# Kernel optimization log

Hardware: AMD Instinct MI355X
Metric: run time of the kernel (lower is better)

## Reference

```python
import jax, jax.numpy as jnp
import numpy as np

B, N, M, K = 4, 16384, 16384, 16   # batch, points, centers, neighbors
C, O, G = 64, 64, 8                # in_planes, out_planes, group


def setup_inputs() -> dict:
    key = jax.random.key(0)
    ks = jax.random.split(key, 16)
    r = lambda i, sh, s=1.0: jax.random.normal(ks[i], sh, jnp.float32) * s
    return dict(
        center_pos=r(0, (B, M, 3)),
        center_fea=r(1, (B, C, M)),
        pos=r(2, (B, N, 3)),
        fea=r(3, (B, C, N)),
        idx=jax.random.randint(ks[4], (B, M, K), 0, N, jnp.int32),
        # linear q/k/v
        Wq=r(5, (C, O), 0.05), bq=jnp.zeros((O,), jnp.float32),
        Wk=r(6, (C, O), 0.05), bk=jnp.zeros((O,), jnp.float32),
        Wv=r(7, (C, O), 0.05), bv=jnp.zeros((O,), jnp.float32),
        # center_pos_encode: conv1x1(3->O, no bias) + folded BN (scale,shift) + relu + conv1x1(O->O)
        cpe_w1=r(8, (3, O), 0.05), cpe_s=jnp.ones((O,), jnp.float32), cpe_b=jnp.zeros((O,), jnp.float32),
        cpe_w2=r(9, (O, O), 0.05), cpe_b2=jnp.zeros((O,), jnp.float32),
        # pos_encode (Conv2d 1x1 == per-point linear)
        pe_w1=r(10, (3, O), 0.05), pe_s=jnp.ones((O,), jnp.float32), pe_b=jnp.zeros((O,), jnp.float32),
        pe_w2=r(11, (O, O), 0.05), pe_b2=jnp.zeros((O,), jnp.float32),
        # weight_encode (O -> G)
        we_w1=r(12, (O, G), 0.05), we_s=jnp.ones((G,), jnp.float32), we_b=jnp.zeros((G,), jnp.float32),
        we_w2=r(13, (G, G), 0.05), we_b2=jnp.zeros((G,), jnp.float32),
    )


def _mlp2(x, w1, s, b, w2, b2):
    # conv1x1(no bias) -> inference BatchNorm folded to (scale, shift) -> ReLU -> conv1x1(+bias)
    h = jax.nn.relu(x @ w1 * s + b)
    return h @ w2 + b2


def reference(center_pos, center_fea, pos, fea, idx,
              Wq, bq, Wk, bk, Wv, bv,
              cpe_w1, cpe_s, cpe_b, cpe_w2, cpe_b2,
              pe_w1, pe_s, pe_b, pe_w2, pe_b2,
              we_w1, we_s, we_b, we_w2, we_b2):
    x_q = center_fea.transpose(0, 2, 1) @ Wq + bq        # [B,M,O]
    ft = fea.transpose(0, 2, 1)                          # [B,N,C]
    x_k = ft @ Wk + bk                                   # [B,N,O]
    x_v = ft @ Wv + bv                                   # [B,N,O]

    gather = jax.vmap(lambda a, i: a[i])                 # per-batch irregular gather
    nk = gather(x_k, idx)                                # [B,M,K,O]
    nv = gather(x_v, idx)                                # [B,M,K,O]
    npos = gather(pos, idx) - center_pos[:, :, None, :]  # [B,M,K,3] relative coords

    cpr = _mlp2(center_pos, cpe_w1, cpe_s, cpe_b, cpe_w2, cpe_b2)  # [B,M,O]
    pr = _mlp2(npos, pe_w1, pe_s, pe_b, pe_w2, pe_b2)              # [B,M,K,O]

    r_qk = nk - x_q[:, :, None, :] + cpr[:, :, None, :]  # [B,M,K,O]
    v = nv + pr                                          # [B,M,K,O]

    w = _mlp2(r_qk, we_w1, we_s, we_b, we_w2, we_b2)     # [B,M,K,G]
    w = jax.nn.softmax(w, axis=2)                        # softmax over neighbors

    v = v.reshape(B, M, K, G, O // G)
    out = jnp.einsum('bmkgi,bmkg->bmgi', v, w).reshape(B, M, O)
    return out.transpose(0, 2, 1)                        # [B,O,M]
```

## Files before the change

kernel.cpp:

```cpp
#include <hip/hip_runtime.h>
#include <hip/hip_bf16.h>

typedef unsigned short u16;
typedef __attribute__((ext_vector_type(8))) __bf16 bf8v;
typedef __attribute__((ext_vector_type(4))) float f32x4;
typedef __attribute__((ext_vector_type(4))) unsigned uint4v;

#define B_ 4
#define N_ 16384
#define M_ 16384
#define K_ 16
#define C_ 64
#define O_ 64
#define G_ 8

__device__ __forceinline__ float bf2f(u16 x){
  union { unsigned u; float f; } v; v.u = ((unsigned)x) << 16; return v.f;
}
__device__ __forceinline__ u16 f2bf(float f){
  union { float f; unsigned u; } v; v.f = f;
  unsigned u = v.u;
  return (u16)((u + 0x7FFFu + ((u >> 16) & 1u)) >> 16);
}

__global__ __launch_bounds__(256) void pre_kernel(
    const float* __restrict__ center_pos, const float* __restrict__ center_fea,
    const float* __restrict__ fea,
    const float* __restrict__ Wq, const float* __restrict__ bq,
    const float* __restrict__ Wk, const float* __restrict__ bk,
    const float* __restrict__ Wv, const float* __restrict__ bv,
    const float* __restrict__ cpe_w1, const float* __restrict__ cpe_s, const float* __restrict__ cpe_b,
    const float* __restrict__ cpe_w2, const float* __restrict__ cpe_b2,
    const float* __restrict__ we_w1,
    u16* __restrict__ xk, u16* __restrict__ xv, float* __restrict__ qw)
{
  int tid = threadIdx.x;
  int blk = blockIdx.x;
  __shared__ u16 sWT[128*72];
  __shared__ u16 sOut[64*136];
  __shared__ float sMisc[784];

  int l = tid & 63, w = tid >> 6, c = l & 15, q = l >> 4;

  if (blk < 1024) {
    int P0 = blk * 64; int b = P0 >> 14; int n0 = P0 & (N_-1);
    for (int e = tid; e < 8192; e += 256){
      int k = e >> 7, col = e & 127;
      float v = (col < 64) ? Wk[k*64 + col] : Wv[k*64 + (col-64)];
      sWT[col*72 + k] = f2bf(v);
    }
    if (tid < 128) sMisc[tid] = (tid < 64) ? bk[tid] : bv[tid-64];
    __syncthreads();

    int mIdx = n0 + w*16 + c;
    const float* fb = fea + (long)b*C_*N_;
    bf8v af[2];
    #pragma unroll
    for (int ks=0; ks<2; ks++){
      union { bf8v v; u16 s[8]; } ua;
      #pragma unroll
      for (int j=0; j<8; j++)
        ua.s[j] = f2bf(fb[(long)(ks*32 + q*8 + j)*N_ + mIdx]);
      af[ks] = ua.v;
    }

    f32x4 acc[8];
    #pragma unroll
    for (int t=0; t<8; t++){
      float bias = sMisc[16*t + c];
      f32x4 a_ = {bias, bias, bias, bias};
      bf8v b0 = *(const bf8v*)&sWT[(16*t + c)*72 + q*8];
      bf8v b1 = *(const bf8v*)&sWT[(16*t + c)*72 + 32 + q*8];
      a_ = __builtin_amdgcn_mfma_f32_16x16x32_bf16(af[0], b0, a_, 0,0,0);
      a_ = __builtin_amdgcn_mfma_f32_16x16x32_bf16(af[1], b1, a_, 0,0,0);
      acc[t] = a_;
    }

    #pragma unroll
    for (int t=0; t<8; t++)
      #pragma unroll
      for (int r=0; r<4; r++)
        sOut[(w*16 + q*4 + r)*136 + 16*t + c] = f2bf(acc[t][r]);
    __syncthreads();

    #pragma unroll
    for (int rep=0; rep<4; rep++){
      int chunk = rep*256 + tid;
      int pt = chunk >> 4, c8i = chunk & 15;
      uint4v val = *(const uint4v*)&sOut[pt*136 + c8i*8];
      int col8 = c8i*8;
      long row = (long)P0 + pt;
      if (col8 < 64) *(uint4v*)(xk + row*64 + col8)      = val;
      else           *(uint4v*)(xv + row*64 + (col8-64)) = val;
    }
  } else {
    int P0 = (blk - 1024) * 64; int b = P0 >> 14; int m0 = P0 & (M_-1);
    for (int e = tid; e < 512; e += 256) sMisc[e] = we_w1[e];
    if (tid < 64){
      float sc = cpe_s[tid];
      sMisc[512+tid] = cpe_w1[tid]      * sc;
      sMisc[576+tid] = cpe_w1[64+tid]   * sc;
      sMisc[640+tid] = cpe_w1[128+tid]  * sc;
      sMisc[704+tid] = cpe_b[tid];
    }
    __syncthreads();

    {
      int k = tid >> 1, g0 = (tid & 1)*4;
      const float* brow = (k < 64) ? (cpe_w2 + k*64) : (Wq + (k-64)*64);
      float sgn = (k < 64) ? 1.f : -1.f;
      float aw[4] = {0.f,0.f,0.f,0.f};
      for (int o=0; o<64; o++){
        float bo = brow[o]*sgn;
        #pragma unroll
        for (int gg=0; gg<4; gg++) aw[gg] += bo * sMisc[o*8 + g0+gg];
      }
      #pragma unroll
      for (int gg=0; gg<4; gg++) sWT[(g0+gg)*136 + k] = f2bf(aw[gg]);
    }
    for (int e = tid; e < 1088; e += 256) sWT[1088 + e] = 0;
    if (tid < 8){
      float s = 0.f;
      for (int o=0; o<64; o++) s += (cpe_b2[o] - bq[o]) * sMisc[o*8 + tid];
      sMisc[768 + tid] = s;
    }
    __syncthreads();

    int pg = P0 + w*16 + c;
    int mIdx = m0 + w*16 + c;
    long c3 = (long)pg * 3;
    float cp0 = center_pos[c3], cp1 = center_pos[c3+1], cp2 = center_pos[c3+2];
    bf8v ah[2], acf[2];
    #pragma unroll
    for (int ks=0; ks<2; ks++){
      union { bf8v v; u16 s[8]; } ua;
      #pragma unroll
      for (int j=0; j<8; j++){
        int h = ks*32 + q*8 + j;
        float hv = cp0*sMisc[512+h] + cp1*sMisc[576+h] + cp2*sMisc[640+h] + sMisc[704+h];
        ua.s[j] = f2bf(fmaxf(hv, 0.f));
      }
      ah[ks] = ua.v;
    }
    const float* cfb = center_fea + (long)b*C_*M_;
    #pragma unroll
    for (int ks=0; ks<2; ks++){
      union { bf8v v; u16 s[8]; } ua;
      #pragma unroll
      for (int j=0; j<8; j++)
        ua.s[j] = f2bf(cfb[(long)(ks*32 + q*8 + j)*M_ + mIdx]);
      acf[ks] = ua.v;
    }

    float cinit = (c < 8) ? sMisc[768 + c] : 0.f;
    f32x4 aq = {cinit, cinit, cinit, cinit};
    {
      bf8v b0 = *(const bf8v*)&sWT[c*136 + q*8];
      bf8v b1 = *(const bf8v*)&sWT[c*136 + 32 + q*8];
      bf8v b2 = *(const bf8v*)&sWT[c*136 + 64 + q*8];
      bf8v b3 = *(const bf8v*)&sWT[c*136 + 96 + q*8];
      aq = __builtin_amdgcn_mfma_f32_16x16x32_bf16(ah[0], b0, aq, 0,0,0);
      aq = __builtin_amdgcn_mfma_f32_16x16x32_bf16(ah[1], b1, aq, 0,0,0);
      aq = __builtin_amdgcn_mfma_f32_16x16x32_bf16(acf[0], b2, aq, 0,0,0);
      aq = __builtin_amdgcn_mfma_f32_16x16x32_bf16(acf[1], b3, aq, 0,0,0);
    }
    __syncthreads();
    if (c < 8){
      #pragma unroll
      for (int r=0; r<4; r++) sMisc[(w*16 + q*4 + r)*8 + c] = aq[r];
    }
    __syncthreads();
    for (int e = tid; e < 512; e += 256)
      qw[(long)P0*8 + e] = sMisc[e];
  }
}

__global__ __launch_bounds__(256) void attn_kernel(
    const float* __restrict__ center_pos, const float* __restrict__ pos,
    const int* __restrict__ idx,
    const float* __restrict__ pe_w1, const float* __restrict__ pe_s, const float* __restrict__ pe_b,
    const float* __restrict__ pe_w2, const float* __restrict__ pe_b2,
    const float* __restrict__ we_w1, const float* __restrict__ we_s, const float* __restrict__ we_b,
    const float* __restrict__ we_w2, const float* __restrict__ we_b2,
    const u16* __restrict__ xk, const u16* __restrict__ xv, const float* __restrict__ qw,
    float* __restrict__ out)
{
  int tid = threadIdx.x;
  __shared__ float s_w1f[192];
  __shared__ float s_pb[64];
  __shared__ float s_ws[8], s_wb[8], s_wb2[8];
  __shared__ float s_ww2[64];
  __shared__ float s_pb2[64];
  __shared__ u16  s_vt[4*16*72];
  __shared__ float s_tile[32*66];

  if (tid < 64){
    float sc = pe_s[tid];
    s_w1f[tid]     = pe_w1[tid]*sc;
    s_w1f[64+tid]  = pe_w1[64+tid]*sc;
    s_w1f[128+tid] = pe_w1[128+tid]*sc;
    s_pb[tid]  = pe_b[tid];
    s_pb2[tid] = pe_b2[tid];
    s_ww2[tid] = we_w2[tid];
  }
  if (tid >= 64 && tid < 72){
    int g = tid-64;
    s_ws[g]=we_s[g]; s_wb[g]=we_b[g]; s_wb2[g]=we_b2[g];
  }
  __syncthreads();

  int w = tid >> 6, l = tid & 63, c = l & 15, q = l >> 4, c8 = c & 7, qb = l & 48;

  bf8v pw2f[4][2], ww1f[2];
  {
    union { bf8v v; u16 s[8]; } u_;
    #pragma unroll
    for (int t=0;t<4;t++)
      #pragma unroll
      for (int ks=0;ks<2;ks++){
        #pragma unroll
        for (int j=0;j<8;j++) u_.s[j] = f2bf(pe_w2[(ks*32 + q*8 + j)*64 + t*16 + c]);
        pw2f[t][ks] = u_.v;
      }
    #pragma unroll
    for (int ks=0;ks<2;ks++){
      #pragma unroll
      for (int j=0;j<8;j++) u_.s[j] = (c < 8) ? f2bf(we_w1[(ks*32 + q*8 + j)*8 + c]) : (u16)0;
      ww1f[ks] = u_.v;
    }
  }
  float ws_c = s_ws[c8], wb_c = s_wb[c8], wb2_c = s_wb2[c8];
  float w2col[8];
  #pragma unroll
  for (int g=0; g<8; g++) w2col[g] = s_ww2[g*8 + c8];
  float pb2t[4];
  #pragma unroll
  for (int t=0;t<4;t++) pb2t[t] = s_pb2[t*16 + c];

  int pbase = blockIdx.x * 32;
  int b = pbase >> 14;
  long xkb = (long)b * N_ * 64;
  u16* vt = s_vt + w*(16*72);

  int p = pbase + w*8;
  int iv = idx[(long)p*16 + c];
  float qpv = qw[(long)p*8 + c8];
  long c30 = (long)p*3;
  float cp0 = center_pos[c30], cp1 = center_pos[c30+1], cp2 = center_pos[c30+2];

  #pragma unroll 1
  for (int i = 0; i < 8; i++){
    long pr3 = ((long)b*N_ + iv) * 3;
    float np0 = pos[pr3]   - cp0;
    float np1 = pos[pr3+1] - cp1;
    float np2 = pos[pr3+2] - cp2;
    const u16* krow = xk + xkb + (long)iv * 64;
    bf8v ka0 = *(const bf8v*)(krow + q*8);
    bf8v ka1 = *(const bf8v*)(krow + 32 + q*8);
    const u16* vrow = xv + xkb + (long)iv * 64;
    uint4v va0 = *(const uint4v*)(vrow + q*8);
    uint4v va1 = *(const uint4v*)(vrow + 32 + q*8);

    int pn = p + ((i < 7) ? 1 : 0);
    int iv_n = idx[(long)pn*16 + c];
    float qpv_n = qw[(long)pn*8 + c8];
    long c3n = (long)pn*3;
    float cpn0 = center_pos[c3n], cpn1 = center_pos[c3n+1], cpn2 = center_pos[c3n+2];

    *(uint4v*)&vt[c*72 + q*8]      = va0;
    *(uint4v*)&vt[c*72 + 32 + q*8] = va1;

    bf8v h1f[2];
    {
      union { bf8v v; u16 s[8]; } hu;
      #pragma unroll
      for (int ks=0;ks<2;ks++){
        #pragma unroll
        for (int j=0;j<8;j++){
          int o = ks*32 + q*8 + j;
          float hv = np0*s_w1f[o] + np1*s_w1f[64+o] + np2*s_w1f[128+o] + s_pb[o];
          hu.s[j] = f2bf(fmaxf(hv, 0.f));
        }
        h1f[ks] = hu.v;
      }
    }

    f32x4 h2a = {qpv, qpv, qpv, qpv};
    h2a = __builtin_amdgcn_mfma_f32_16x16x32_bf16(ka0, ww1f[0], h2a, 0, 0, 0);
    h2a = __builtin_amdgcn_mfma_f32_16x16x32_bf16(ka1, ww1f[1], h2a, 0, 0, 0);

    f32x4 prA[4];
    #pragma unroll
    for (int t=0;t<4;t++){
      f32x4 z = {0.f,0.f,0.f,0.f};
      z = __builtin_amdgcn_mfma_f32_16x16x32_bf16(h1f[0], pw2f[t][0], z, 0, 0, 0);
      z = __builtin_amdgcn_mfma_f32_16x16x32_bf16(h1f[1], pw2f[t][1], z, 0, 0, 0);
      prA[t] = z;
    }

    float h2r[4];
    #pragma unroll
    for (int r=0;r<4;r++) h2r[r] = fmaxf(h2a[r]*ws_c + wb_c, 0.f);
    float wl[4] = {wb2_c, wb2_c, wb2_c, wb2_c};
    #pragma unroll
    for (int g=0; g<8; g++){
      float wg = w2col[g];
      #pragma unroll
      for (int r=0;r<4;r++)
        wl[r] += __shfl(h2r[r], qb | g, 64) * wg;
    }
    float mx = fmaxf(fmaxf(wl[0],wl[1]), fmaxf(wl[2],wl[3]));
    mx = fmaxf(mx, __shfl_xor(mx, 16, 64));
    mx = fmaxf(mx, __shfl_xor(mx, 32, 64));
    float e[4];
    #pragma unroll
    for (int r=0;r<4;r++) e[r] = exp2f((wl[r]-mx)*1.44269504f);
    float sm = e[0]+e[1]+e[2]+e[3];
    sm += __shfl_xor(sm, 16, 64);
    sm += __shfl_xor(sm, 32, 64);
    float rn = 1.0f / sm;
    #pragma unroll
    for (int r=0;r<4;r++) e[r] *= rn;

    float ov[4] = {0.f,0.f,0.f,0.f};
    int ch = c >> 3;
    #pragma unroll
    for (int r=0;r<4;r++){
      #pragma unroll
      for (int t=0;t<4;t++){
        float wv_ = __shfl(e[r], qb | (t*2 + ch), 64);
        float nvv = bf2f(vt[(q*4+r)*72 + t*16 + c]);
        ov[t] += (prA[t][r] + nvv) * wv_;
      }
    }
    #pragma unroll
    for (int t=0;t<4;t++){
      ov[t] += __shfl_xor(ov[t], 16, 64);
      ov[t] += __shfl_xor(ov[t], 32, 64);
      ov[t] += pb2t[t];
    }
    float selv = ov[0];
    selv = (q==1) ? ov[1] : selv;
    selv = (q==2) ? ov[2] : selv;
    selv = (q==3) ? ov[3] : selv;
    s_tile[(w*8+i)*66 + l] = selv;

    p = pn; iv = iv_n; qpv = qpv_n; cp0 = cpn0; cp1 = cpn1; cp2 = cpn2;
  }
  __syncthreads();

  int o0 = tid >> 5, pt = tid & 31;
  int m0 = pbase & (M_-1);
  long outb = ((long)b*64) * M_ + m0 + pt;
  #pragma unroll
  for (int ii=0; ii<8; ii++){
    int o = o0*8 + ii;
    out[outb + (long)o*M_] = s_tile[pt*66 + o];
  }
}

extern "C" void kernel_launch(void* const* d_in, const int* in_sizes, int n_in,
                              void* d_out, int out_size, void* d_ws, size_t ws_size,
                              hipStream_t stream) {
  const float* center_pos = (const float*)d_in[0];
  const float* center_fea = (const float*)d_in[1];
  const float* pos        = (const float*)d_in[2];
  const float* fea        = (const float*)d_in[3];
  const int*   idx        = (const int*)d_in[4];
  const float* Wq = (const float*)d_in[5];   const float* bq = (const float*)d_in[6];
  const float* Wk = (const float*)d_in[7];   const float* bk = (const float*)d_in[8];
  const float* Wv = (const float*)d_in[9];   const float* bv = (const float*)d_in[10];
  const float* cpe_w1 = (const float*)d_in[11]; const float* cpe_s = (const float*)d_in[12];
  const float* cpe_b  = (const float*)d_in[13]; const float* cpe_w2 = (const float*)d_in[14];
  const float* cpe_b2 = (const float*)d_in[15];
  const float* pe_w1 = (const float*)d_in[16]; const float* pe_s = (const float*)d_in[17];
  const float* pe_b  = (const float*)d_in[18]; const float* pe_w2 = (const float*)d_in[19];
  const float* pe_b2 = (const float*)d_in[20];
  const float* we_w1 = (const float*)d_in[21]; const float* we_s = (const float*)d_in[22];
  const float* we_b  = (const float*)d_in[23]; const float* we_w2 = (const float*)d_in[24];
  const float* we_b2 = (const float*)d_in[25];

  const size_t SZ = (size_t)B_*N_*64;
  u16* xk = (u16*)d_ws;
  u16* xv = xk + SZ;
  float* qwp = (float*)(xv + SZ);
  float* outp = (float*)d_out;

  hipLaunchKernelGGL(pre_kernel, dim3(2048), dim3(256), 0, stream,
      center_pos, center_fea, fea, Wq, bq, Wk, bk, Wv, bv,
      cpe_w1, cpe_s, cpe_b, cpe_w2, cpe_b2, we_w1, xk, xv, qwp);
  hipLaunchKernelGGL(attn_kernel, dim3(2048), dim3(256), 0, stream,
      center_pos, pos, idx, pe_w1, pe_s, pe_b, pe_w2, pe_b2,
      we_w1, we_s, we_b, we_w2, we_b2, xk, xv, qwp, outp);
}
```

Before: 225.8 us.

## Split pre-kernel, coalesce feature loads via LDS, and process two centers per attention iteration

```diff
diff --git a/kernel.cpp b/kernel.cpp
--- a/kernel.cpp
+++ b/kernel.cpp
@@ -22,160 +22,179 @@
   unsigned u = v.u;
   return (u16)((u + 0x7FFFu + ((u >> 16) & 1u)) >> 16);
 }
-
-__global__ __launch_bounds__(256) void pre_kernel(
-    const float* __restrict__ center_pos, const float* __restrict__ center_fea,
+union pk2 { unsigned u; _Float16 h[2]; };
+__device__ __forceinline__ unsigned packh(float a, float b){
+  pk2 p; p.h[0] = (_Float16)a; p.h[1] = (_Float16)b; return p.u;
+}
+
+__global__ __launch_bounds__(256) void setup_kernel(
+    const float* __restrict__ Wq, const float* __restrict__ bq,
+    const float* __restrict__ cpe_w2, const float* __restrict__ cpe_b2,
+    const float* __restrict__ we_w1,
+    u16* __restrict__ bw, float* __restrict__ cinit)
+{
+  __shared__ float sWe[512];
+  int tid = threadIdx.x;
+  for (int e = tid; e < 512; e += 256) sWe[e] = we_w1[e];
+  __syncthreads();
+  int k = tid >> 1, g0 = (tid & 1)*4;
+  const float* brow = (k < 64) ? (cpe_w2 + k*64) : (Wq + (k-64)*64);
+  float sgn = (k < 64) ? 1.f : -1.f;
+  float aw[4] = {0.f,0.f,0.f,0.f};
+  for (int o = 0; o < 64; o++){
+    float bo = brow[o]*sgn;
+    #pragma unroll
+    for (int gg=0; gg<4; gg++) aw[gg] += bo * sWe[o*8 + g0+gg];
+  }
+  #pragma unroll
+  for (int gg=0; gg<4; gg++) bw[(g0+gg)*136 + k] = f2bf(aw[gg]);
+  for (int e = tid; e < 2176; e += 256){
+    int r = e / 136, cc = e % 136;
+    if (r >= 8 || cc >= 128) bw[e] = 0;
+  }
+  if (tid < 8){
+    float s = 0.f;
+    for (int o = 0; o < 64; o++) s += (cpe_b2[o] - bq[o]) * sWe[o*8 + tid];
+    cinit[tid] = s;
+  }
+}
+
+__global__ __launch_bounds__(256) void kv_kernel(
     const float* __restrict__ fea,
-    const float* __restrict__ Wq, const float* __restrict__ bq,
     const float* __restrict__ Wk, const float* __restrict__ bk,
     const float* __restrict__ Wv, const float* __restrict__ bv,
+    u16* __restrict__ xk, u16* __restrict__ xv)
+{
+  __shared__ u16 sWT[128*72];
+  __shared__ u16 sA[64*72];
+  __shared__ u16 sOut[64*136];
+  __shared__ float sBias[128];
+  int tid = threadIdx.x;
+  int l = tid & 63, w = tid >> 6, c = l & 15, q = l >> 4;
+  int P0 = blockIdx.x * 64; int b = P0 >> 14; int n0 = P0 & (N_-1);
+  const float* fb = fea + (long)b*C_*N_;
+
+  #pragma unroll
+  for (int pp = 0; pp < 4; pp++){
+    int k = pp*16 + (tid >> 4);
+    int nf = (tid & 15)*4;
+    f32x4 v = *(const f32x4*)&fb[(long)k*N_ + n0 + nf];
+    sA[(nf+0)*72+k] = f2bf(v[0]); sA[(nf+1)*72+k] = f2bf(v[1]);
+    sA[(nf+2)*72+k] = f2bf(v[2]); sA[(nf+3)*72+k] = f2bf(v[3]);
+  }
+  for (int e = tid; e < 8192; e += 256){
+    int k = e >> 7, col = e & 127;
+    float v = (col < 64) ? Wk[k*64 + col] : Wv[k*64 + (col-64)];
+    sWT[col*72 + k] = f2bf(v);
+  }
+  if (tid < 128) sBias[tid] = (tid < 64) ? bk[tid] : bv[tid-64];
+  __syncthreads();
+
+  bf8v af0 = *(const bf8v*)&sA[(w*16+c)*72 + q*8];
+  bf8v af1 = *(const bf8v*)&sA[(w*16+c)*72 + 32 + q*8];
+
+  f32x4 acc[8];
+  #pragma unroll
+  for (int t = 0; t < 8; t++){
+    float bias = sBias[16*t + c];
+    f32x4 a_ = {bias, bias, bias, bias};
+    bf8v b0 = *(const bf8v*)&sWT[(16*t + c)*72 + q*8];
+    bf8v b1 = *(const bf8v*)&sWT[(16*t + c)*72 + 32 + q*8];
+    a_ = __builtin_amdgcn_mfma_f32_16x16x32_bf16(af0, b0, a_, 0,0,0);
+    a_ = __builtin_amdgcn_mfma_f32_16x16x32_bf16(af1, b1, a_, 0,0,0);
+    acc[t] = a_;
+  }
+  #pragma unroll
+  for (int t = 0; t < 8; t++)
+    #pragma unroll
+    for (int r = 0; r < 4; r++)
+      sOut[(w*16 + q*4 + r)*136 + 16*t + c] = f2bf(acc[t][r]);
+  __syncthreads();
+
+  #pragma unroll
+  for (int rep = 0; rep < 4; rep++){
+    int chunk = rep*256 + tid;
+    int pt = chunk >> 4, c8i = chunk & 15;
+    uint4v val = *(const uint4v*)&sOut[pt*136 + c8i*8];
+    int col8 = c8i*8;
+    long row = (long)P0 + pt;
+    if (col8 < 64) *(uint4v*)(xk + row*64 + col8)      = val;
+    else           *(uint4v*)(xv + row*64 + (col8-64)) = val;
+  }
+}
+
+__global__ __launch_bounds__(256) void qc_kernel(
+    const float* __restrict__ center_pos, const float* __restrict__ center_fea,
     const float* __restrict__ cpe_w1, const float* __restrict__ cpe_s, const float* __restrict__ cpe_b,
-    const float* __restrict__ cpe_w2, const float* __restrict__ cpe_b2,
-    const float* __restrict__ we_w1,
-    u16* __restrict__ xk, u16* __restrict__ xv, float* __restrict__ qw)
+    const u16* __restrict__ bw, const float* __restrict__ cinit,
+    float* __restrict__ qw)
 {
+  __shared__ u16 sBw[16*136];
+  __shared__ u16 sA[64*72];
+  __shared__ float sW1[256];
+  __shared__ float sQ[512];
   int tid = threadIdx.x;
-  int blk = blockIdx.x;
-  __shared__ u16 sWT[128*72];
-  __shared__ u16 sOut[64*136];
-  __shared__ float sMisc[784];
-
   int l = tid & 63, w = tid >> 6, c = l & 15, q = l >> 4;
-
-  if (blk < 1024) {
-    int P0 = blk * 64; int b = P0 >> 14; int n0 = P0 & (N_-1);
-    for (int e = tid; e < 8192; e += 256){
-      int k = e >> 7, col = e & 127;
-      float v = (col < 64) ? Wk[k*64 + col] : Wv[k*64 + (col-64)];
-      sWT[col*72 + k] = f2bf(v);
-    }
-    if (tid < 128) sMisc[tid] = (tid < 64) ? bk[tid] : bv[tid-64];
-    __syncthreads();
-
-    int mIdx = n0 + w*16 + c;
-    const float* fb = fea + (long)b*C_*N_;
-    bf8v af[2];
-    #pragma unroll
-    for (int ks=0; ks<2; ks++){
-      union { bf8v v; u16 s[8]; } ua;
-      #pragma unroll
-      for (int j=0; j<8; j++)
-        ua.s[j] = f2bf(fb[(long)(ks*32 + q*8 + j)*N_ + mIdx]);
-      af[ks] = ua.v;
-    }
-
-    f32x4 acc[8];
-    #pragma unroll
-    for (int t=0; t<8; t++){
-      float bias = sMisc[16*t + c];
-      f32x4 a_ = {bias, bias, bias, bias};
-      bf8v b0 = *(const bf8v*)&sWT[(16*t + c)*72 + q*8];
-      bf8v b1 = *(const bf8v*)&sWT[(16*t + c)*72 + 32 + q*8];
-      a_ = __builtin_amdgcn_mfma_f32_16x16x32_bf16(af[0], b0, a_, 0,0,0);
-      a_ = __builtin_amdgcn_mfma_f32_16x16x32_bf16(af[1], b1, a_, 0,0,0);
-      acc[t] = a_;
-    }
-
-    #pragma unroll
-    for (int t=0; t<8; t++)
-      #pragma unroll
-      for (int r=0; r<4; r++)
-        sOut[(w*16 + q*4 + r)*136 + 16*t + c] = f2bf(acc[t][r]);
-    __syncthreads();
-
-    #pragma unroll
-    for (int rep=0; rep<4; rep++){
-      int chunk = rep*256 + tid;
-      int pt = chunk >> 4, c8i = chunk & 15;
-      uint4v val = *(const uint4v*)&sOut[pt*136 + c8i*8];
-      int col8 = c8i*8;
-      long row = (long)P0 + pt;
-      if (col8 < 64) *(uint4v*)(xk + row*64 + col8)      = val;
-      else           *(uint4v*)(xv + row*64 + (col8-64)) = val;
-    }
-  } else {
-    int P0 = (blk - 1024) * 64; int b = P0 >> 14; int m0 = P0 & (M_-1);
-    for (int e = tid; e < 512; e += 256) sMisc[e] = we_w1[e];
-    if (tid < 64){
-      float sc = cpe_s[tid];
-      sMisc[512+tid] = cpe_w1[tid]      * sc;
-      sMisc[576+tid] = cpe_w1[64+tid]   * sc;
-      sMisc[640+tid] = cpe_w1[128+tid]  * sc;
-      sMisc[704+tid] = cpe_b[tid];
-    }
-    __syncthreads();
-
-    {
-      int k = tid >> 1, g0 = (tid & 1)*4;
-      const float* brow = (k < 64) ? (cpe_w2 + k*64) : (Wq + (k-64)*64);
-      float sgn = (k < 64) ? 1.f : -1.f;
-      float aw[4] = {0.f,0.f,0.f,0.f};
-      for (int o=0; o<64; o++){
-        float bo = brow[o]*sgn;
-        #pragma unroll
-        for (int gg=0; gg<4; gg++) aw[gg] += bo * sMisc[o*8 + g0+gg];
-      }
-      #pragma unroll
-      for (int gg=0; gg<4; gg++) sWT[(g0+gg)*136 + k] = f2bf(aw[gg]);
-    }
-    for (int e = tid; e < 1088; e += 256) sWT[1088 + e] = 0;
-    if (tid < 8){
-      float s = 0.f;
-      for (int o=0; o<64; o++) s += (cpe_b2[o] - bq[o]) * sMisc[o*8 + tid];
-      sMisc[768 + tid] = s;
-    }
-    __syncthreads();
-
-    int pg = P0 + w*16 + c;
-    int mIdx = m0 + w*16 + c;
-    long c3 = (long)pg * 3;
-    float cp0 = center_pos[c3], cp1 = center_pos[c3+1], cp2 = center_pos[c3+2];
-    bf8v ah[2], acf[2];
-    #pragma unroll
-    for (int ks=0; ks<2; ks++){
-      union { bf8v v; u16 s[8]; } ua;
-      #pragma unroll
-      for (int j=0; j<8; j++){
-        int h = ks*32 + q*8 + j;
-        float hv = cp0*sMisc[512+h] + cp1*sMisc[576+h] + cp2*sMisc[640+h] + sMisc[704+h];
-        ua.s[j] = f2bf(fmaxf(hv, 0.f));
-      }
-      ah[ks] = ua.v;
-    }
-    const float* cfb = center_fea + (long)b*C_*M_;
-    #pragma unroll
-    for (int ks=0; ks<2; ks++){
-      union { bf8v v; u16 s[8]; } ua;
-      #pragma unroll
-      for (int j=0; j<8; j++)
-        ua.s[j] = f2bf(cfb[(long)(ks*32 + q*8 + j)*M_ + mIdx]);
-      acf[ks] = ua.v;
-    }
-
-    float cinit = (c < 8) ? sMisc[768 + c] : 0.f;
-    f32x4 aq = {cinit, cinit, cinit, cinit};
-    {
-      bf8v b0 = *(const bf8v*)&sWT[c*136 + q*8];
-      bf8v b1 = *(const bf8v*)&sWT[c*136 + 32 + q*8];
-      bf8v b2 = *(const bf8v*)&sWT[c*136 + 64 + q*8];
-      bf8v b3 = *(const bf8v*)&sWT[c*136 + 96 + q*8];
-      aq = __builtin_amdgcn_mfma_f32_16x16x32_bf16(ah[0], b0, aq, 0,0,0);
-      aq = __builtin_amdgcn_mfma_f32_16x16x32_bf16(ah[1], b1, aq, 0,0,0);
-      aq = __builtin_amdgcn_mfma_f32_16x16x32_bf16(acf[0], b2, aq, 0,0,0);
-      aq = __builtin_amdgcn_mfma_f32_16x16x32_bf16(acf[1], b3, aq, 0,0,0);
-    }
-    __syncthreads();
-    if (c < 8){
-      #pragma unroll
-      for (int r=0; r<4; r++) sMisc[(w*16 + q*4 + r)*8 + c] = aq[r];
-    }
-    __syncthreads();
-    for (int e = tid; e < 512; e += 256)
-      qw[(long)P0*8 + e] = sMisc[e];
-  }
-}
-
-__global__ __launch_bounds__(256) void attn_kernel(
+  int P0 = blockIdx.x * 64; int b = P0 >> 14; int m0 = P0 & (M_-1);
+  const float* cfb = center_fea + (long)b*C_*M_;
+
+  #pragma unroll
+  for (int pp = 0; pp < 4; pp++){
+    int k = pp*16 + (tid >> 4);
+    int nf = (tid & 15)*4;
+    f32x4 v = *(const f32x4*)&cfb[(long)k*M_ + m0 + nf];
+    sA[(nf+0)*72+k] = f2bf(v[0]); sA[(nf+1)*72+k] = f2bf(v[1]);
+    sA[(nf+2)*72+k] = f2bf(v[2]); sA[(nf+3)*72+k] = f2bf(v[3]);
+  }
+  for (int e = tid; e < 2176; e += 256) sBw[e] = bw[e];
+  if (tid < 64){
+    float sc = cpe_s[tid];
+    sW1[tid]     = cpe_w1[tid]*sc;
+    sW1[64+tid]  = cpe_w1[64+tid]*sc;
+    sW1[128+tid] = cpe_w1[128+tid]*sc;
+    sW1[192+tid] = cpe_b[tid];
+  }
+  long c3 = (long)(P0 + w*16 + c)*3;
+  float cp0 = center_pos[c3], cp1 = center_pos[c3+1], cp2 = center_pos[c3+2];
+  __syncthreads();
+
+  bf8v ah[2], acf[2];
+  #pragma unroll
+  for (int ks = 0; ks < 2; ks++){
+    union { bf8v v; u16 sv[8]; } ua;
+    #pragma unroll
+    for (int j = 0; j < 8; j++){
+      int h = ks*32 + q*8 + j;
+      float hv = cp0*sW1[h] + cp1*sW1[64+h] + cp2*sW1[128+h] + sW1[192+h];
+      ua.sv[j] = f2bf(fmaxf(hv, 0.f));
+    }
+    ah[ks] = ua.v;
+  }
+  acf[0] = *(const bf8v*)&sA[(w*16+c)*72 + q*8];
+  acf[1] = *(const bf8v*)&sA[(w*16+c)*72 + 32 + q*8];
+
+  float ci = (c < 8) ? cinit[c] : 0.f;
+  f32x4 aq = {ci, ci, ci, ci};
+  {
+    bf8v b0 = *(const bf8v*)&sBw[c*136 + q*8];
+    bf8v b1 = *(const bf8v*)&sBw[c*136 + 32 + q*8];
+    bf8v b2 = *(const bf8v*)&sBw[c*136 + 64 + q*8];
+    bf8v b3 = *(const bf8v*)&sBw[c*136 + 96 + q*8];
+    aq = __builtin_amdgcn_mfma_f32_16x16x32_bf16(ah[0],  b0, aq, 0,0,0);
+    aq = __builtin_amdgcn_mfma_f32_16x16x32_bf16(ah[1],  b1, aq, 0,0,0);
+    aq = __builtin_amdgcn_mfma_f32_16x16x32_bf16(acf[0], b2, aq, 0,0,0);
+    aq = __builtin_amdgcn_mfma_f32_16x16x32_bf16(acf[1], b3, aq, 0,0,0);
+  }
+  if (c < 8){
+    #pragma unroll
+    for (int r = 0; r < 4; r++) sQ[(w*16 + q*4 + r)*8 + c] = aq[r];
+  }
+  __syncthreads();
+  for (int e = tid; e < 512; e += 256)
+    qw[(long)P0*8 + e] = sQ[e];
+}
+
+__global__ __launch_bounds__(256, 3) void attn_kernel(
     const float* __restrict__ center_pos, const float* __restrict__ pos,
     const int* __restrict__ idx,
     const float* __restrict__ pe_w1, const float* __restrict__ pe_s, const float* __restrict__ pe_b,
@@ -186,12 +205,10 @@
     float* __restrict__ out)
 {
   int tid = threadIdx.x;
-  __shared__ float s_w1f[192];
-  __shared__ float s_pb[64];
-  __shared__ float s_ws[8], s_wb[8], s_wb2[8];
-  __shared__ float s_ww2[64];
-  __shared__ float s_pb2[64];
-  __shared__ u16  s_vt[4*16*72];
+  __shared__ float s_w1f[192], s_pb[64], s_pb2[64], s_ww2[64];
+  __shared__ float s_ws8[8], s_wb8[8], s_wb28[8];
+  __shared__ u16  s_stage[64*72 + 16*72];
+  __shared__ u16  s_vt[4*2*16*72];
   __shared__ float s_tile[32*66];
 
   if (tid < 64){
@@ -205,147 +222,191 @@
   }
   if (tid >= 64 && tid < 72){
     int g = tid-64;
-    s_ws[g]=we_s[g]; s_wb[g]=we_b[g]; s_wb2[g]=we_b2[g];
-  }
+    s_ws8[g]=we_s[g]; s_wb8[g]=we_b[g]; s_wb28[g]=we_b2[g];
+  }
+  #pragma unroll
+  for (int pp = 0; pp < 4; pp++){
+    int row = pp*16 + (tid >> 4);
+    int colf = (tid & 15)*4;
+    f32x4 v = *(const f32x4*)&pe_w2[row*64 + colf];
+    s_stage[(colf+0)*72+row] = f2bf(v[0]); s_stage[(colf+1)*72+row] = f2bf(v[1]);
+    s_stage[(colf+2)*72+row] = f2bf(v[2]); s_stage[(colf+3)*72+row] = f2bf(v[3]);
+  }
+  u16* s2 = s_stage + 64*72;
+  for (int e = tid; e < 512; e += 256){
+    int k = e >> 3, cc = e & 7;
+    s2[cc*72 + k] = f2bf(we_w1[e]);
+  }
+  for (int e = tid; e < 576; e += 256) s2[576 + e] = 0;
   __syncthreads();
 
   int w = tid >> 6, l = tid & 63, c = l & 15, q = l >> 4, c8 = c & 7, qb = l & 48;
 
   bf8v pw2f[4][2], ww1f[2];
-  {
-    union { bf8v v; u16 s[8]; } u_;
-    #pragma unroll
-    for (int t=0;t<4;t++)
-      #pragma unroll
-      for (int ks=0;ks<2;ks++){
-        #pragma unroll
-        for (int j=0;j<8;j++) u_.s[j] = f2bf(pe_w2[(ks*32 + q*8 + j)*64 + t*16 + c]);
-        pw2f[t][ks] = u_.v;
-      }
-    #pragma unroll
-    for (int ks=0;ks<2;ks++){
-      #pragma unroll
-      for (int j=0;j<8;j++) u_.s[j] = (c < 8) ? f2bf(we_w1[(ks*32 + q*8 + j)*8 + c]) : (u16)0;
-      ww1f[ks] = u_.v;
-    }
-  }
-  float ws_c = s_ws[c8], wb_c = s_wb[c8], wb2_c = s_wb2[c8];
+  #pragma unroll
+  for (int t = 0; t < 4; t++){
+    pw2f[t][0] = *(const bf8v*)&s_stage[(t*16+c)*72 + q*8];
+    pw2f[t][1] = *(const bf8v*)&s_stage[(t*16+c)*72 + 32 + q*8];
+  }
+  ww1f[0] = *(const bf8v*)&s2[c*72 + q*8];
+  ww1f[1] = *(const bf8v*)&s2[c*72 + 32 + q*8];
+
+  float ws_c = s_ws8[c8], wb_c = s_wb8[c8], wb2_c = s_wb28[c8];
   float w2col[8];
   #pragma unroll
-  for (int g=0; g<8; g++) w2col[g] = s_ww2[g*8 + c8];
+  for (int g = 0; g < 8; g++) w2col[g] = s_ww2[g*8 + c8];
   float pb2t[4];
   #pragma unroll
-  for (int t=0;t<4;t++) pb2t[t] = s_pb2[t*16 + c];
+  for (int t = 0; t < 4; t++) pb2t[t] = s_pb2[t*16 + c];
 
   int pbase = blockIdx.x * 32;
   int b = pbase >> 14;
   long xkb = (long)b * N_ * 64;
-  u16* vt = s_vt + w*(16*72);
-
-  int p = pbase + w*8;
-  int iv = idx[(long)p*16 + c];
-  float qpv = qw[(long)p*8 + c8];
-  long c30 = (long)p*3;
-  float cp0 = center_pos[c30], cp1 = center_pos[c30+1], cp2 = center_pos[c30+2];
+  u16* vt0 = s_vt + w*(2*16*72);
+  u16* vt1 = vt0 + 16*72;
+  int ch = c >> 3;
+
+  int pb0 = pbase + w*8;
+  int iv0 = idx[(long)pb0*16 + c];
+  int iv1 = idx[(long)(pb0+1)*16 + c];
+  float qp0 = qw[(long)pb0*8 + c8];
+  float qp1 = qw[(long)(pb0+1)*8 + c8];
+  long c30 = (long)pb0*3, c31 = (long)(pb0+1)*3;
+  float cpA0 = center_pos[c30], cpA1 = center_pos[c30+1], cpA2 = center_pos[c30+2];
+  float cpB0 = center_pos[c31], cpB1 = center_pos[c31+1], cpB2 = center_pos[c31+2];
 
   #pragma unroll 1
-  for (int i = 0; i < 8; i++){
-    long pr3 = ((long)b*N_ + iv) * 3;
-    float np0 = pos[pr3]   - cp0;
-    float np1 = pos[pr3+1] - cp1;
-    float np2 = pos[pr3+2] - cp2;
-    const u16* krow = xk + xkb + (long)iv * 64;
-    bf8v ka0 = *(const bf8v*)(krow + q*8);
-    bf8v ka1 = *(const bf8v*)(krow + 32 + q*8);
-    const u16* vrow = xv + xkb + (long)iv * 64;
-    uint4v va0 = *(const uint4v*)(vrow + q*8);
-    uint4v va1 = *(const uint4v*)(vrow + 32 + q*8);
-
-    int pn = p + ((i < 7) ? 1 : 0);
-    int iv_n = idx[(long)pn*16 + c];
-    float qpv_n = qw[(long)pn*8 + c8];
-    long c3n = (long)pn*3;
-    float cpn0 = center_pos[c3n], cpn1 = center_pos[c3n+1], cpn2 = center_pos[c3n+2];
-
-    *(uint4v*)&vt[c*72 + q*8]      = va0;
-    *(uint4v*)&vt[c*72 + 32 + q*8] = va1;
-
-    bf8v h1f[2];
-    {
-      union { bf8v v; u16 s[8]; } hu;
+  for (int i = 0; i < 4; i++){
+    long prA = ((long)b*N_ + iv0)*3, prB = ((long)b*N_ + iv1)*3;
+    float pxA = pos[prA], pyA = pos[prA+1], pzA = pos[prA+2];
+    float pxB = pos[prB], pyB = pos[prB+1], pzB = pos[prB+2];
+    const u16* kr0 = xk + xkb + (long)iv0*64;
+    const u16* kr1 = xk + xkb + (long)iv1*64;
+    bf8v ka00 = *(const bf8v*)(kr0 + q*8),  ka01 = *(const bf8v*)(kr0 + 32 + q*8);
+    bf8v ka10 = *(const bf8v*)(kr1 + q*8),  ka11 = *(const bf8v*)(kr1 + 32 + q*8);
+    const u16* vr0 = xv + xkb + (long)iv0*64;
+    const u16* vr1 = xv + xkb + (long)iv1*64;
+    uint4v va00 = *(const uint4v*)(vr0 + q*8), va01 = *(const uint4v*)(vr0 + 32 + q*8);
+    uint4v va10 = *(const uint4v*)(vr1 + q*8), va11 = *(const uint4v*)(vr1 + 32 + q*8);
+
+    int p2 = pb0 + ((i < 3) ? 2*i + 2 : 2*i);
+    int p3 = p2 + 1;
+    int ivn0 = idx[(long)p2*16 + c];
+    int ivn1 = idx[(long)p3*16 + c];
+    float qpn0 = qw[(long)p2*8 + c8];
+    float qpn1 = qw[(long)p3*8 + c8];
+    long c3n0 = (long)p2*3, c3n1 = (long)p3*3;
+    float cpnA0 = center_pos[c3n0], cpnA1 = center_pos[c3n0+1], cpnA2 = center_pos[c3n0+2];
+    float cpnB0 = center_pos[c3n1], cpnB1 = center_pos[c3n1+1], cpnB2 = center_pos[c3n1+2];
+
+    *(uint4v*)&vt0[c*72 + q*8]      = va00;
+    *(uint4v*)&vt0[c*72 + 32 + q*8] = va01;
+    *(uint4v*)&vt1[c*72 + q*8]      = va10;
+    *(uint4v*)&vt1[c*72 + 32 + q*8] = va11;
+
+    float npA0 = pxA - cpA0, npA1 = pyA - cpA1, npA2 = pzA - cpA2;
+    float npB0 = pxB - cpB0, npB1 = pyB - cpB1, npB2 = pzB - cpB2;
+    bf8v h1A[2], h1B[2];
+    #pragma unroll
+    for (int ks = 0; ks < 2; ks++){
+      union { bf8v v; u16 s[8]; } ha, hb;
       #pragma unroll
-      for (int ks=0;ks<2;ks++){
-        #pragma unroll
-        for (int j=0;j<8;j++){
-          int o = ks*32 + q*8 + j;
-          float hv = np0*s_w1f[o] + np1*s_w1f[64+o] + np2*s_w1f[128+o] + s_pb[o];
-          hu.s[j] = f2bf(fmaxf(hv, 0.f));
-        }
-        h1f[ks] = hu.v;
+      for (int j = 0; j < 8; j++){
+        int o = ks*32 + q*8 + j;
+        float w1 = s_w1f[o], w2 = s_w1f[64+o], w3 = s_w1f[128+o], bb = s_pb[o];
+        ha.s[j] = f2bf(fmaxf(npA0*w1 + npA1*w2 + npA2*w3 + bb, 0.f));
+        hb.s[j] = f2bf(fmaxf(npB0*w1 + npB1*w2 + npB2*w3 + bb, 0.f));
       }
-    }
-
-    f32x4 h2a = {qpv, qpv, qpv, qpv};
-    h2a = __builtin_amdgcn_mfma_f32_16x16x32_bf16(ka0, ww1f[0], h2a, 0, 0, 0);
-    h2a = __builtin_amdgcn_mfma_f32_16x16x32_bf16(ka1, ww1f[1], h2a, 0, 0, 0);
-
-    f32x4 prA[4];
-    #pragma unroll
-    for (int t=0;t<4;t++){
-      f32x4 z = {0.f,0.f,0.f,0.f};
-      z = __builtin_amdgcn_mfma_f32_16x16x32_bf16(h1f[0], pw2f[t][0], z, 0, 0, 0);
-      z = __builtin_amdgcn_mfma_f32_16x16x32_bf16(h1f[1], pw2f[t][1], z, 0, 0, 0);
-      prA[t] = z;
-    }
-
-    float h2r[4];
-    #pragma unroll
-    for (int r=0;r<4;r++) h2r[r] = fmaxf(h2a[r]*ws_c + wb_c, 0.f);
-    float wl[4] = {wb2_c, wb2_c, wb2_c, wb2_c};
-    #pragma unroll
-    for (int g=0; g<8; g++){
+      h1A[ks] = ha.v; h1B[ks] = hb.v;
+    }
+
+    f32x4 h2a0 = {qp0, qp0, qp0, qp0};
+    f32x4 h2a1 = {qp1, qp1, qp1, qp1};
+    h2a0 = __builtin_amdgcn_mfma_f32_16x16x32_bf16(ka00, ww1f[0], h2a0, 0,0,0);
+    h2a1 = __builtin_amdgcn_mfma_f32_16x16x32_bf16(ka10, ww1f[0], h2a1, 0,0,0);
+    h2a0 = __builtin_amdgcn_mfma_f32_16x16x32_bf16(ka01, ww1f[1], h2a0, 0,0,0);
+    h2a1 = __builtin_amdgcn_mfma_f32_16x16x32_bf16(ka11, ww1f[1], h2a1, 0,0,0);
+
+    float h2r0[4], h2r1[4];
+    #pragma unroll
+    for (int r = 0; r < 4; r++){
+      h2r0[r] = fmaxf(h2a0[r]*ws_c + wb_c, 0.f);
+      h2r1[r] = fmaxf(h2a1[r]*ws_c + wb_c, 0.f);
+    }
+    unsigned hp00 = packh(h2r0[0], h2r0[1]), hp01 = packh(h2r0[2], h2r0[3]);
+    unsigned hp10 = packh(h2r1[0], h2r1[1]), hp11 = packh(h2r1[2], h2r1[3]);
+    float wl0[4] = {wb2_c, wb2_c, wb2_c, wb2_c};
+    float wl1[4] = {wb2_c, wb2_c, wb2_c, wb2_c};
+    #pragma unroll
+    for (int g = 0; g < 8; g++){
       float wg = w2col[g];
-      #pragma unroll
-      for (int r=0;r<4;r++)
-        wl[r] += __shfl(h2r[r], qb | g, 64) * wg;
-    }
-    float mx = fmaxf(fmaxf(wl[0],wl[1]), fmaxf(wl[2],wl[3]));
-    mx = fmaxf(mx, __shfl_xor(mx, 16, 64));
-    mx = fmaxf(mx, __shfl_xor(mx, 32, 64));
-    float e[4];
-    #pragma unroll
-    for (int r=0;r<4;r++) e[r] = exp2f((wl[r]-mx)*1.44269504f);
-    float sm = e[0]+e[1]+e[2]+e[3];
-    sm += __shfl_xor(sm, 16, 64);
-    sm += __shfl_xor(sm, 32, 64);
-    float rn = 1.0f / sm;
-    #pragma unroll
-    for (int r=0;r<4;r++) e[r] *= rn;
-
-    float ov[4] = {0.f,0.f,0.f,0.f};
-    int ch = c >> 3;
-    #pragma unroll
-    for (int r=0;r<4;r++){
-      #pragma unroll
-      for (int t=0;t<4;t++){
-        float wv_ = __shfl(e[r], qb | (t*2 + ch), 64);
-        float nvv = bf2f(vt[(q*4+r)*72 + t*16 + c]);
-        ov[t] += (prA[t][r] + nvv) * wv_;
-      }
-    }
-    #pragma unroll
-    for (int t=0;t<4;t++){
-      ov[t] += __shfl_xor(ov[t], 16, 64);
-      ov[t] += __shfl_xor(ov[t], 32, 64);
-      ov[t] += pb2t[t];
-    }
-    float selv = ov[0];
-    selv = (q==1) ? ov[1] : selv;
-    selv = (q==2) ? ov[2] : selv;
-    selv = (q==3) ? ov[3] : selv;
-    s_tile[(w*8+i)*66 + l] = selv;
-
-    p = pn; iv = iv_n; qpv = qpv_n; cp0 = cpn0; cp1 = cpn1; cp2 = cpn2;
+      pk2 a0; a0.u = (unsigned)__shfl((int)hp00, qb | g, 64);
+      pk2 a1; a1.u = (unsigned)__shfl((int)hp01, qb | g, 64);
+      pk2 b0; b0.u = (unsigned)__shfl((int)hp10, qb | g, 64);
+      pk2 b1; b1.u = (unsigned)__shfl((int)hp11, qb | g, 64);
+      wl0[0] += (float)a0.h[0]*wg; wl0[1] += (float)a0.h[1]*wg;
+      wl0[2] += (float)a1.h[0]*wg; wl0[3] += (float)a1.h[1]*wg;
+      wl1[0] += (float)b0.h[0]*wg; wl1[1] += (float)b0.h[1]*wg;
+      wl1[2] += (float)b1.h[0]*wg; wl1[3] += (float)b1.h[1]*wg;
+    }
+    float e0[4], e1[4];
+    #pragma unroll
+    for (int r = 0; r < 4; r++){
+      e0[r] = exp2f(wl0[r]*1.44269504f);
+      e1[r] = exp2f(wl1[r]*1.44269504f);
+    }
+    float sm0 = e0[0]+e0[1]+e0[2]+e0[3];
+    float sm1 = e1[0]+e1[1]+e1[2]+e1[3];
+    sm0 += __shfl_xor(sm0, 16, 64); sm1 += __shfl_xor(sm1, 16, 64);
+    sm0 += __shfl_xor(sm0, 32, 64); sm1 += __shfl_xor(sm1, 32, 64);
+    float rn0 = 1.0f/sm0, rn1 = 1.0f/sm1;
+    #pragma unroll
+    for (int r = 0; r < 4; r++){ e0[r] *= rn0; e1[r] *= rn1; }
+    unsigned ep00 = packh(e0[0], e0[1]), ep01 = packh(e0[2], e0[3]);
+    unsigned ep10 = packh(e1[0], e1[1]), ep11 = packh(e1[2], e1[3]);
+
+    float ov0[4], ov1[4];
+    #pragma unroll
+    for (int t = 0; t < 4; t++){
+      f32x4 z0 = {0.f,0.f,0.f,0.f}, z1 = {0.f,0.f,0.f,0.f};
+      z0 = __builtin_amdgcn_mfma_f32_16x16x32_bf16(h1A[0], pw2f[t][0], z0, 0,0,0);
+      z1 = __builtin_amdgcn_mfma_f32_16x16x32_bf16(h1B[0], pw2f[t][0], z1, 0,0,0);
+      z0 = __builtin_amdgcn_mfma_f32_16x16x32_bf16(h1A[1], pw2f[t][1], z0, 0,0,0);
+      z1 = __builtin_amdgcn_mfma_f32_16x16x32_bf16(h1B[1], pw2f[t][1], z1, 0,0,0);
+      int src = qb | (t*2 + ch);
+      pk2 wA0; wA0.u = (unsigned)__shfl((int)ep00, src, 64);
+      pk2 wA1; wA1.u = (unsigned)__shfl((int)ep01, src, 64);
+      pk2 wB0; wB0.u = (unsigned)__shfl((int)ep10, src, 64);
+      pk2 wB1; wB1.u = (unsigned)__shfl((int)ep11, src, 64);
+      float a = 0.f, bacc = 0.f;
+      a += (z0[0] + bf2f(vt0[(q*4+0)*72 + t*16 + c])) * (float)wA0.h[0];
+      a += (z0[1] + bf2f(vt0[(q*4+1)*72 + t*16 + c])) * (float)wA0.h[1];
+      a += (z0[2] + bf2f(vt0[(q*4+2)*72 + t*16 + c])) * (float)wA1.h[0];
+      a += (z0[3] + bf2f(vt0[(q*4+3)*72 + t*16 + c])) * (float)wA1.h[1];
+      bacc += (z1[0] + bf2f(vt1[(q*4+0)*72 + t*16 + c])) * (float)wB0.h[0];
+      bacc += (z1[1] + bf2f(vt1[(q*4+1)*72 + t*16 + c])) * (float)wB0.h[1];
+      bacc += (z1[2] + bf2f(vt1[(q*4+2)*72 + t*16 + c])) * (float)wB1.h[0];
+      bacc += (z1[3] + bf2f(vt1[(q*4+3)*72 + t*16 + c])) * (float)wB1.h[1];
+      ov0[t] = a; ov1[t] = bacc;
+    }
+    #pragma unroll
+    for (int t = 0; t < 4; t++){
+      ov0[t] += __shfl_xor(ov0[t], 16, 64);
+      ov1[t] += __shfl_xor(ov1[t], 16, 64);
+      ov0[t] += __shfl_xor(ov0[t], 32, 64);
+      ov1[t] += __shfl_xor(ov1[t], 32, 64);
+      ov0[t] += pb2t[t]; ov1[t] += pb2t[t];
+    }
+    float s0 = ov0[0], s1 = ov1[0];
+    s0 = (q==1) ? ov0[1] : s0;  s1 = (q==1) ? ov1[1] : s1;
+    s0 = (q==2) ? ov0[2] : s0;  s1 = (q==2) ? ov1[2] : s1;
+    s0 = (q==3) ? ov0[3] : s0;  s1 = (q==3) ? ov1[3] : s1;
+    s_tile[(w*8 + 2*i + 0)*66 + l] = s0;
+    s_tile[(w*8 + 2*i + 1)*66 + l] = s1;
+
+    iv0 = ivn0; iv1 = ivn1; qp0 = qpn0; qp1 = qpn1;
+    cpA0 = cpnA0; cpA1 = cpnA1; cpA2 = cpnA2;
+    cpB0 = cpnB0; cpB1 = cpnB1; cpB2 = cpnB2;
   }
   __syncthreads();
 
@@ -353,7 +414,7 @@
   int m0 = pbase & (M_-1);
   long outb = ((long)b*64) * M_ + m0 + pt;
   #pragma unroll
-  for (int ii=0; ii<8; ii++){
+  for (int ii = 0; ii < 8; ii++){
     int o = o0*8 + ii;
     out[outb + (long)o*M_] = s_tile[pt*66 + o];
   }
@@ -384,11 +445,16 @@
   u16* xk = (u16*)d_ws;
   u16* xv = xk + SZ;
   float* qwp = (float*)(xv + SZ);
+  u16* bwp = (u16*)(qwp + (size_t)B_*M_*8);
+  float* cinitp = (float*)(bwp + 2176);
   float* outp = (float*)d_out;
 
-  hipLaunchKernelGGL(pre_kernel, dim3(2048), dim3(256), 0, stream,
-      center_pos, center_fea, fea, Wq, bq, Wk, bk, Wv, bv,
-      cpe_w1, cpe_s, cpe_b, cpe_w2, cpe_b2, we_w1, xk, xv, qwp);
+  hipLaunchKernelGGL(setup_kernel, dim3(1), dim3(256), 0, stream,
+      Wq, bq, cpe_w2, cpe_b2, we_w1, bwp, cinitp);
+  hipLaunchKernelGGL(kv_kernel, dim3(1024), dim3(256), 0, stream,
+      fea, Wk, bk, Wv, bv, xk, xv);
+  hipLaunchKernelGGL(qc_kernel, dim3(1024), dim3(256), 0, stream,
+      center_pos, center_fea, cpe_w1, cpe_s, cpe_b, bwp, cinitp, qwp);
   hipLaunchKernelGGL(attn_kernel, dim3(2048), dim3(256), 0, stream,
       center_pos, pos, idx, pe_w1, pe_s, pe_b, pe_w2, pe_b2,
       we_w1, we_s, we_b, we_w2, we_b2, xk, xv, qwp, outp);
```

Measured after the change: 309.4 us. 1.37x slower.
